# Kernel tuning notes

Hardware: AMD Instinct MI355X
Metric: run time of the kernel (lower is better)

Reference implementation:

```python
import jax, jax.numpy as jnp
import numpy as np

B, C, H, W = 8, 256, 128, 128
N = H * W
TEMP = 0.07
NUM_NEG = 128
HARD_RADIUS = 4
HARD_RATIO = 0.75   # curriculum fully ramped (_current_hard_ratio == hard_ratio_max)
N_HARD = int(NUM_NEG * HARD_RATIO)   # 96
N_RAND = NUM_NEG - N_HARD            # 32
STEP = max(1, H // 16)               # 8
N_POS = ((H + STEP - 1) // STEP) * ((W + STEP - 1) // STEP)  # 256


def setup_inputs() -> dict:
    key = jax.random.key(0)
    ks = jax.random.split(key, 8)
    fmap_rgb = jax.random.normal(ks[0], (B, C, H, W), jnp.float32)
    fmap_depth = jax.random.normal(ks[1], (B, C, H, W), jnp.float32)
    pu = jax.random.uniform(ks[2], (B, H, W), jnp.float32) * (W - 1)
    pv = jax.random.uniform(ks[3], (B, H, W), jnp.float32) * (H - 1)
    projected_coords = jnp.stack([pu, pv], axis=1)  # (B,2,H,W)
    valid_mask = (jax.random.uniform(ks[4], (B, H, W)) < 0.9).astype(jnp.float32)
    rand_idx = jax.random.randint(ks[5], (B, N_RAND), 0, N, dtype=jnp.int32)
    hard_off_u = jax.random.randint(ks[6], (B, N_HARD, N_POS), -HARD_RADIUS, HARD_RADIUS + 1, dtype=jnp.int32)
    hard_off_v = jax.random.randint(ks[7], (B, N_HARD, N_POS), -HARD_RADIUS, HARD_RADIUS + 1, dtype=jnp.int32)
    return {
        'fmap_rgb': fmap_rgb, 'fmap_depth': fmap_depth,
        'projected_coords': projected_coords, 'valid_mask': valid_mask,
        'rand_idx': rand_idx, 'hard_off_u': hard_off_u, 'hard_off_v': hard_off_v,
    }


def _normalize(x):
    # F.normalize(dim=1): x / max(||x||_2, eps)
    n = jnp.sqrt(jnp.sum(x * x, axis=1, keepdims=True))
    return x / jnp.maximum(n, 1e-12)


def _bilinear_sample(f, x, y):
    # grid_sample(mode=bilinear, padding=zeros, align_corners=True); unnormalized
    # coords equal pixel coords (x=proj_u, y=proj_v). f:(B,C,H,W), x,y:(B,H,W) -> (B,C,N)
    Bb, Cc, Hh, Ww = f.shape
    ff = f.reshape(Bb, Cc, Hh * Ww)
    xf = x.reshape(Bb, -1)
    yf = y.reshape(Bb, -1)
    x0 = jnp.floor(xf)
    y0 = jnp.floor(yf)
    wx = xf - x0
    wy = yf - y0
    x0i = x0.astype(jnp.int32)
    y0i = y0.astype(jnp.int32)

    def g(ix, iy):
        valid = (ix >= 0) & (ix < Ww) & (iy >= 0) & (iy < Hh)
        idx = jnp.clip(iy, 0, Hh - 1) * Ww + jnp.clip(ix, 0, Ww - 1)
        v = jnp.take_along_axis(ff, idx[:, None, :], axis=2)
        return v * valid[:, None, :]

    return (((1 - wx) * (1 - wy))[:, None, :] * g(x0i, y0i)
            + (wx * (1 - wy))[:, None, :] * g(x0i + 1, y0i)
            + ((1 - wx) * wy)[:, None, :] * g(x0i, y0i + 1)
            + (wx * wy)[:, None, :] * g(x0i + 1, y0i + 1))


def reference(fmap_rgb, fmap_depth, projected_coords, valid_mask, rand_idx, hard_off_u, hard_off_v):
    rgb = _normalize(fmap_rgb)
    dep = _normalize(fmap_depth)
    proj_u = projected_coords[:, 0]
    proj_v = projected_coords[:, 1]

    rgb_pos = _bilinear_sample(rgb, proj_u, proj_v)        # (B,C,N)
    dep_flat = dep.reshape(B, C, N)
    rgb_flat = rgb.reshape(B, C, N)
    pos_sim = jnp.sum(dep_flat * rgb_pos, axis=1) / TEMP    # (B,N)

    # random negatives via gather + batched matmul
    rgb_rand = jnp.take_along_axis(rgb_flat, rand_idx[:, None, :].astype(jnp.int32), axis=2)  # (B,C,n_rand)
    rand_neg = jnp.einsum('bcn,bck->bkn', dep_flat, rgb_rand) / TEMP  # (B,n_rand,N)

    # hard negatives on coarse grid (step = H//16)
    gh = jnp.arange(0, H, STEP)
    gw = jnp.arange(0, W, STEP)
    ghf, gwf = [a.reshape(-1) for a in jnp.meshgrid(gh, gw, indexing='ij')]
    grid_idx = ghf * W + gwf                                # (n_pos,)
    pos_u = jnp.clip(proj_u[:, ghf, gwf], 0, W - 1).astype(jnp.int32)  # (B,n_pos)
    pos_v = jnp.clip(proj_v[:, ghf, gwf], 0, H - 1).astype(jnp.int32)
    off_u = jnp.where((hard_off_u == 0) & (hard_off_v == 0), 1, hard_off_u)
    hu = jnp.clip(pos_u[:, None, :] + off_u, 0, W - 1)      # (B,n_hard,n_pos)
    hv = jnp.clip(pos_v[:, None, :] + hard_off_v, 0, H - 1)
    hard_idx = (hv * W + hu).reshape(B, -1)                 # (B, n_hard*n_pos)
    rgb_hard = jnp.take_along_axis(rgb_flat, hard_idx[:, None, :], axis=2).reshape(B, C, N_HARD, N_POS)
    dep_grid = dep_flat[:, :, grid_idx]                     # (B,C,n_pos)
    hard_sim = jnp.einsum('bcp,bchp->bhp', dep_grid, rgb_hard) / TEMP  # (B,n_hard,n_pos)

    # logsumexp over [pos; random negs; hard negs] -- hard negs only exist at grid
    # positions (the torch code scatters into a dense -inf (B,n_hard,N) tensor;
    # logaddexp at grid positions is mathematically identical and avoids it).
    lse_base = jax.scipy.special.logsumexp(
        jnp.concatenate([pos_sim[:, None, :], rand_neg], axis=1), axis=1)  # (B,N)
    lse_hard = jax.scipy.special.logsumexp(hard_sim, axis=1)               # (B,n_pos)
    lse = lse_base.at[:, grid_idx].set(jnp.logaddexp(lse_base[:, grid_idx], lse_hard))

    mask = valid_mask.reshape(B, N)
    denom = jnp.maximum(jnp.sum(mask), 1.0)
    loss = jnp.sum((lse - pos_sim) * mask) / denom

    # accuracy (no_grad in torch); max over all negatives, hard ones only at grid idx
    max_neg = jnp.max(rand_neg, axis=1)
    max_neg = max_neg.at[:, grid_idx].max(jnp.max(hard_sim, axis=1))
    correct = ((pos_sim > max_neg) & (mask > 0.5)).astype(jnp.float32)
    accuracy = jnp.sum(correct) / denom * 100.0
    return loss, jax.lax.stop_gradient(accuracy)
```

## Files before the change

### kernel.cpp

```cpp
#include <hip/hip_runtime.h>
#include <cfloat>
#include <math.h>

#define B_ 8
#define C_ 256
#define C2_ (C_/2)
#define H_ 128
#define W_ 128
#define N_ (H_*W_)
#define NRAND 32
#define NHARD 96
#define NPOS 256
#define INV_TEMP (1.0f/0.07f)

typedef __attribute__((ext_vector_type(8))) short short8;
typedef __attribute__((ext_vector_type(4))) float f32x4;

__device__ __forceinline__ unsigned bf16rne(float x) {
    unsigned u = __float_as_uint(x);
    return (u + 0x7FFFu + ((u >> 16) & 1u)) >> 16;
}
__device__ __forceinline__ float blo(unsigned w) { return __uint_as_float(w << 16); }
__device__ __forceinline__ float bhi(unsigned w) { return __uint_as_float(w & 0xFFFF0000u); }

__global__ __launch_bounds__(256) void k1_rgb_norm_T(const float* __restrict__ rgb,
                                                     unsigned* __restrict__ rgbT) {
    __shared__ float tile[C_][67];
    __shared__ float redx[8][32], redy[8][32];
    __shared__ float invn[64];
    int bi = blockIdx.x;
    int b  = bi >> 8;
    int p0 = (bi & 255) << 6;
    int t  = threadIdx.x;
    int pxh = t & 31;
    int cg  = t >> 5;
    const float2* src2 = (const float2*)(rgb + (size_t)b * C_ * N_);
    float ssx = 0.f, ssy = 0.f;
    #pragma unroll 4
    for (int p = 0; p < 32; ++p) {
        int c = p * 8 + cg;
        float2 v = src2[(size_t)c * (N_ / 2) + (p0 >> 1) + pxh];
        tile[c][2 * pxh]     = v.x;
        tile[c][2 * pxh + 1] = v.y;
        ssx += v.x * v.x;
        ssy += v.y * v.y;
    }
    redx[cg][pxh] = ssx; redy[cg][pxh] = ssy;
    __syncthreads();
    if (t < 32) {
        float sx = 0.f, sy = 0.f;
        #pragma unroll
        for (int g2 = 0; g2 < 8; ++g2) { sx += redx[g2][t]; sy += redy[g2][t]; }
        invn[2 * t]     = 1.0f / fmaxf(sqrtf(sx), 1e-12f);
        invn[2 * t + 1] = 1.0f / fmaxf(sqrtf(sy), 1e-12f);
    }
    __syncthreads();
    unsigned* dst = rgbT + (size_t)(b * N_ + p0) * C2_;
    int u  = t & 127;
    int ph = t >> 7;
    #pragma unroll 4
    for (int it = 0; it < 32; ++it) {
        int px = ph + 2 * it;
        float sc = invn[px];
        unsigned pa = bf16rne(tile[2 * u][px] * sc);
        unsigned pb = bf16rne(tile[2 * u + 1][px] * sc);
        dst[(size_t)px * C2_ + u] = pa | (pb << 16);
    }
}

__global__ __launch_bounds__(256) void k2_main(
        const float* __restrict__ dep, const unsigned* __restrict__ rgbT,
        const float* __restrict__ coords, const int* __restrict__ rand_idx,
        float* __restrict__ lse_base, float* __restrict__ pos_out,
        float* __restrict__ maxneg_out, unsigned* __restrict__ depG) {
    __shared__ __align__(16) uint4 dep4[64 * 32];
    __shared__ __align__(16) uint4 rs4[32 * 32];
    __shared__ float red[4][64];
    __shared__ float invn[64];
    int bi = blockIdx.x;
    int b  = bi >> 8;
    int p0 = (bi & 255) << 6;
    int t  = threadIdx.x;
    int lane = t & 63, w = t >> 6;

    #pragma unroll
    for (int it = 0; it < 4; ++it) {
        int flat = it * 256 + t;
        int rn = flat >> 5, c8 = flat & 31;
        int idx = rand_idx[b * NRAND + rn];
        const uint4* src = (const uint4*)(rgbT + (size_t)(b * N_ + idx) * C2_);
        rs4[rn * 32 + (c8 ^ (rn & 7))] = src[c8];
    }

    const float* depb = dep + (size_t)b * C_ * N_ + p0 + lane;
    float ssq = 0.f;
    int psw = lane & 7;
    #pragma unroll 2
    for (int i = 0; i < 8; ++i) {
        int c0 = w * 64 + i * 8;
        float v[8];
        #pragma unroll
        for (int k = 0; k < 8; ++k) {
            v[k] = depb[(size_t)(c0 + k) * N_];
            ssq += v[k] * v[k];
        }
        uint4 q;
        q.x = bf16rne(v[0]) | (bf16rne(v[1]) << 16);
        q.y = bf16rne(v[2]) | (bf16rne(v[3]) << 16);
        q.z = bf16rne(v[4]) | (bf16rne(v[5]) << 16);
        q.w = bf16rne(v[6]) | (bf16rne(v[7]) << 16);
        dep4[lane * 32 + ((w * 8 + i) ^ psw)] = q;
    }
    red[w][lane] = ssq;

    int px = t >> 2, g = t & 3;
    int n  = p0 + px;
    float xf = coords[(size_t)b * 2 * N_ + n];
    float yf = coords[(size_t)b * 2 * N_ + N_ + n];
    float x0 = floorf(xf), y0 = floorf(yf);
    float wx = xf - x0, wy = yf - y0;
    int ix = (int)x0 + (g & 1);
    int iy = (int)y0 + (g >> 1);
    float wgt = ((g & 1) ? wx : 1.f - wx) * ((g & 2) ? wy : 1.f - wy);
    if (ix < 0 || ix >= W_ || iy < 0 || iy >= H_) wgt = 0.f;
    int ixc = min(max(ix, 0), W_ - 1), iyc = min(max(iy, 0), H_ - 1);
    const uint4* nbr4 = (const uint4*)(rgbT + (size_t)(b * N_ + iyc * W_ + ixc) * C2_);

    __syncthreads();
    if (t < 64) {
        float s = red[0][t] + red[1][t] + red[2][t] + red[3][t];
        invn[t] = 1.0f / fmaxf(sqrtf(s), 1e-12f);
    }

    f32x4 acc0 = {0.f, 0.f, 0.f, 0.f};
    f32x4 acc1 = {0.f, 0.f, 0.f, 0.f};
    int l15 = lane & 15, l4 = lane >> 4;
    int pxA = (w << 4) + l15;
    const short8* lds8 = (const short8*)dep4;
    const short8* rnd8 = (const short8*)rs4;
    #pragma unroll
    for (int kc = 0; kc < 8; ++kc) {
        int c8 = kc * 4 + l4;
        short8 a  = lds8[pxA * 32 + (c8 ^ (pxA & 7))];
        short8 b0 = rnd8[l15 * 32 + (c8 ^ (l15 & 7))];
        short8 b1 = rnd8[(16 + l15) * 32 + (c8 ^ (l15 & 7))];
        acc0 = __builtin_amdgcn_mfma_f32_16x16x32_bf16(a, b0, acc0, 0, 0, 0);
        acc1 = __builtin_amdgcn_mfma_f32_16x16x32_bf16(a, b1, acc1, 0, 0, 0);
    }

    float accN = 0.f;
    const uint4* drow = dep4 + (size_t)px * 32;
    int dsw = px & 7;
    #pragma unroll 4
    for (int c8 = 0; c8 < 32; ++c8) {
        uint4 dq = drow[c8 ^ dsw];
        uint4 rq = nbr4[c8];
        accN += blo(dq.x) * blo(rq.x) + bhi(dq.x) * bhi(rq.x)
              + blo(dq.y) * blo(rq.y) + bhi(dq.y) * bhi(rq.y)
              + blo(dq.z) * blo(rq.z) + bhi(dq.z) * bhi(rq.z)
              + blo(dq.w) * blo(rq.w) + bhi(dq.w) * bhi(rq.w);
    }
    __syncthreads();

    float* simsF = (float*)rs4;
    #pragma unroll
    for (int r = 0; r < 4; ++r) {
        int prow = (w << 4) + (l4 << 2) + r;
        int swn = r << 2;
        simsF[prow * 32 + (l15 ^ swn)]        = acc0[r];
        simsF[prow * 32 + (16 + (l15 ^ swn))] = acc1[r];
    }
    __syncthreads();

    float scale = invn[px] * INV_TEMP;
    float pp = accN * wgt;
    pp += __shfl_xor(pp, 1, 4);
    pp += __shfl_xor(pp, 2, 4);
    float pos = pp * scale;
    const float4* sf = (const float4*)simsF;
    int fsw = px & 3;
    float4 ra = sf[px * 8 + ((g * 2) ^ fsw)];
    float4 rb = sf[px * 8 + (((g * 2) ^ fsw) ^ 1)];
    float r[8] = {ra.x, ra.y, ra.z, ra.w, rb.x, rb.y, rb.z, rb.w};
    float ml = -FLT_MAX;
    #pragma unroll
    for (int j = 0; j < 8; ++j) { r[j] *= scale; ml = fmaxf(ml, r[j]); }
    ml = fmaxf(ml, __shfl_xor(ml, 1, 4));
    ml = fmaxf(ml, __shfl_xor(ml, 2, 4));
    float mneg = ml;
    float mall = fmaxf(mneg, pos);
    float se = 0.f;
    #pragma unroll
    for (int j = 0; j < 8; ++j) se += expf(r[j] - mall);
    se += __shfl_xor(se, 1, 4);
    se += __shfl_xor(se, 2, 4);
    if (g == 0) {
        float lse = mall + logf(se + expf(pos - mall));
        size_t o = (size_t)b * N_ + n;
        lse_base[o]   = lse;
        pos_out[o]    = pos;
        maxneg_out[o] = mneg;
    }

    int y = p0 >> 7;
    if ((y & 7) == 0) {
        int m = t >> 5, u = t & 31;
        int gpx = m * 8;
        int gx  = (p0 & 127) + gpx;
        int p   = ((y >> 3) << 4) + (gx >> 3);
        float sc = invn[gpx];
        const unsigned* srow = (const unsigned*)(dep4 + (size_t)gpx * 32);
        int xsw = (gpx & 7) << 2;
        unsigned* dst = depG + (size_t)((b << 8) + p) * 128;
        #pragma unroll
        for (int it = 0; it < 4; ++it) {
            int uu = u + it * 32;
            unsigned wv = srow[uu ^ xsw];
            dst[uu] = bf16rne(blo(wv) * sc) | (bf16rne(bhi(wv) * sc) << 16);
        }
    }
}

__global__ __launch_bounds__(128) void k3_hard(
        const unsigned* __restrict__ depG, const unsigned* __restrict__ rgbT,
        const float* __restrict__ coords, const int* __restrict__ hoffu,
        const int* __restrict__ hoffv, float* __restrict__ lse_hard,
        float* __restrict__ max_hard) {
    __shared__ __align__(16) float dv[256];
    __shared__ float sm_[2], ss_[2];
    int bp = blockIdx.x;
    int b = bp >> 8, p = bp & 255;
    int gy = (p >> 4) * 8, gx = (p & 15) * 8;
    int nn = gy * W_ + gx;
    int t  = threadIdx.x;
    unsigned wv = depG[(size_t)bp * 128 + t];
    dv[2 * t]     = blo(wv);
    dv[2 * t + 1] = bhi(wv);
    float pu = coords[(size_t)b * 2 * N_ + nn];
    float pv = coords[(size_t)b * 2 * N_ + N_ + nn];
    int iu = (int)fminf(fmaxf(pu, 0.f), (float)(W_ - 1));
    int iv = (int)fminf(fmaxf(pv, 0.f), (float)(H_ - 1));
    float sim = -FLT_MAX;
    int ou = 0, ov = 0;
    if (t < NHARD) {
        ou = hoffu[((size_t)b * NHARD + t) * NPOS + p];
        ov = hoffv[((size_t)b * NHARD + t) * NPOS + p];
    }
    __syncthreads();
    if (t < NHARD) {
        if (ou == 0 && ov == 0) ou = 1;
        int hu = min(max(iu + ou, 0), W_ - 1);
        int hv = min(max(iv + ov, 0), H_ - 1);
        const uint4* hvec = (const uint4*)(rgbT + (size_t)(b * N_ + hv * W_ + hu) * C2_);
        float acc = 0.f;
        #pragma unroll 4
        for (int c8 = 0; c8 < 32; ++c8) {
            uint4 q = hvec[c8];
            float4 d0 = *(const float4*)(&dv[c8 * 8]);
            float4 d1 = *(const float4*)(&dv[c8 * 8 + 4]);
            acc += d0.x * blo(q.x) + d0.y * bhi(q.x)
                 + d0.z * blo(q.y) + d0.w * bhi(q.y)
                 + d1.x * blo(q.z) + d1.y * bhi(q.z)
                 + d1.z * blo(q.w) + d1.w * bhi(q.w);
        }
        sim = acc * INV_TEMP;
    }
    float m = sim;
    #pragma unroll
    for (int o = 32; o > 0; o >>= 1) m = fmaxf(m, __shfl_down(m, o, 64));
    int wid = t >> 6;
    if ((t & 63) == 0) sm_[wid] = m;
    __syncthreads();
    float mm = fmaxf(sm_[0], sm_[1]);
    float e = (t < NHARD) ? expf(sim - mm) : 0.f;
    #pragma unroll
    for (int o = 32; o > 0; o >>= 1) e += __shfl_down(e, o, 64);
    if ((t & 63) == 0) ss_[wid] = e;
    __syncthreads();
    if (t == 0) {
        lse_hard[bp] = mm + logf(ss_[0] + ss_[1]);
        max_hard[bp] = mm;
    }
}

__global__ __launch_bounds__(256) void k4_reduce(
        const float* __restrict__ lse_base, const float* __restrict__ pos_sim,
        const float* __restrict__ max_neg, const float* __restrict__ mask,
        const float* __restrict__ lse_hard, const float* __restrict__ max_hard,
        float* __restrict__ acc) {
    int i = blockIdx.x * 256 + threadIdx.x;
    float l  = lse_base[i], ps = pos_sim[i], mn = max_neg[i], mk = mask[i];
    int b = i >> 14;
    int n = i & (N_ - 1);
    int y = n >> 7, x = n & 127;
    if (((y & 7) | (x & 7)) == 0) {
        int p = ((y >> 3) << 4) + (x >> 3);
        float lh = lse_hard[(b << 8) + p];
        float mh = max_hard[(b << 8) + p];
        float m = fmaxf(l, lh);
        l  = m + logf(expf(l - m) + expf(lh - m));
        mn = fmaxf(mn, mh);
    }
    float s0 = (l - ps) * mk;
    float s1 = (ps > mn && mk > 0.5f) ? 1.f : 0.f;
    float s2 = mk;
    #pragma unroll
    for (int o = 32; o > 0; o >>= 1) {
        s0 += __shfl_down(s0, o, 64);
        s1 += __shfl_down(s1, o, 64);
        s2 += __shfl_down(s2, o, 64);
    }
    __shared__ float r0[4], r1[4], r2[4];
    int wid = threadIdx.x >> 6;
    if ((threadIdx.x & 63) == 0) { r0[wid] = s0; r1[wid] = s1; r2[wid] = s2; }
    __syncthreads();
    if (threadIdx.x == 0) {
        atomicAdd(&acc[0], r0[0] + r0[1] + r0[2] + r0[3]);
        atomicAdd(&acc[1], r1[0] + r1[1] + r1[2] + r1[3]);
        atomicAdd(&acc[2], r2[0] + r2[1] + r2[2] + r2[3]);
    }
}

__global__ void k5_final(const float* __restrict__ acc, float* __restrict__ out) {
    if (threadIdx.x == 0) {
        float denom = fmaxf(acc[2], 1.0f);
        out[0] = acc[0] / denom;
        out[1] = acc[1] / denom * 100.0f;
    }
}

extern "C" void kernel_launch(void* const* d_in, const int* in_sizes, int n_in,
                              void* d_out, int out_size, void* d_ws, size_t ws_size,
                              hipStream_t stream) {
    const float* rgb     = (const float*)d_in[0];
    const float* dep     = (const float*)d_in[1];
    const float* coords  = (const float*)d_in[2];
    const float* mask    = (const float*)d_in[3];
    const int*   rand_i  = (const int*)d_in[4];
    const int*   hoffu   = (const int*)d_in[5];
    const int*   hoffv   = (const int*)d_in[6];
    float* out = (float*)d_out;
    char*  ws  = (char*)d_ws;

    const size_t RGBT_B = (size_t)B_ * N_ * C_ * 2;
    const size_t PIX_B  = (size_t)B_ * N_ * 4;
    unsigned* rgbT  = (unsigned*)ws;
    float* lse_base = (float*)(ws + RGBT_B);
    float* pos_sim  = (float*)(ws + RGBT_B + PIX_B);
    float* max_neg  = (float*)(ws + RGBT_B + 2 * PIX_B);
    float* lse_hard = (float*)(ws + RGBT_B + 3 * PIX_B);
    float* max_hard = (float*)(ws + RGBT_B + 3 * PIX_B + 8192);
    float* acc      = (float*)(ws + RGBT_B + 3 * PIX_B + 2 * 8192);
    unsigned* depG  = (unsigned*)(ws + RGBT_B + 3 * PIX_B + 2 * 8192 + 1024);

    hipMemsetAsync(acc, 0, 16, stream);
    k1_rgb_norm_T<<<B_ * (N_ / 64), 256, 0, stream>>>(rgb, rgbT);
    k2_main<<<B_ * (N_ / 64), 256, 0, stream>>>(dep, rgbT, coords, rand_i,
                                                lse_base, pos_sim, max_neg, depG);
    k3_hard<<<B_ * NPOS, 128, 0, stream>>>(depG, rgbT, coords, hoffu, hoffv,
                                           lse_hard, max_hard);
    k4_reduce<<<(B_ * N_) / 256, 256, 0, stream>>>(lse_base, pos_sim, max_neg,
                                                   mask, lse_hard, max_hard, acc);
    k5_final<<<1, 64, 0, stream>>>(acc, out);
}
```

Before: 370.4 us.

## Register-staged rgb normalize with swizzled LDS transpose; split hard dot over thread pairs

The rgb normalize/transpose kernel now loads 64 channels per thread into registers with coalesced per-channel reads. It packs bf16 pairs into uint4 and stages them through an XOR-swizzled LDS buffer so rows of 16-byte chunks can be written to global memory. This replaces the padded float tile and scalar 4-byte stores. The hard-negative kernel uses 192 threads, with two threads per hard negative each computing half of the 256-channel dot product and combining via a shuffle. That removes the idle lanes of the old 96-of-128 layout and shortens each thread's gather chain, at the cost of heavy register use (64 floats per thread) in k1.

New measurement: 371.8 us. No clear change (+0.4%).

```diff
diff --git a/kernel.cpp b/kernel.cpp
--- a/kernel.cpp
+++ b/kernel.cpp
@@ -25,46 +25,48 @@
 
 __global__ __launch_bounds__(256) void k1_rgb_norm_T(const float* __restrict__ rgb,
                                                      unsigned* __restrict__ rgbT) {
-    __shared__ float tile[C_][67];
-    __shared__ float redx[8][32], redy[8][32];
+    __shared__ __align__(16) uint4 bounce[64 * 32];
+    __shared__ float red[4][64];
     __shared__ float invn[64];
     int bi = blockIdx.x;
     int b  = bi >> 8;
     int p0 = (bi & 255) << 6;
     int t  = threadIdx.x;
-    int pxh = t & 31;
-    int cg  = t >> 5;
-    const float2* src2 = (const float2*)(rgb + (size_t)b * C_ * N_);
-    float ssx = 0.f, ssy = 0.f;
-    #pragma unroll 4
-    for (int p = 0; p < 32; ++p) {
-        int c = p * 8 + cg;
-        float2 v = src2[(size_t)c * (N_ / 2) + (p0 >> 1) + pxh];
-        tile[c][2 * pxh]     = v.x;
-        tile[c][2 * pxh + 1] = v.y;
-        ssx += v.x * v.x;
-        ssy += v.y * v.y;
-    }
-    redx[cg][pxh] = ssx; redy[cg][pxh] = ssy;
-    __syncthreads();
-    if (t < 32) {
-        float sx = 0.f, sy = 0.f;
-        #pragma unroll
-        for (int g2 = 0; g2 < 8; ++g2) { sx += redx[g2][t]; sy += redy[g2][t]; }
-        invn[2 * t]     = 1.0f / fmaxf(sqrtf(sx), 1e-12f);
-        invn[2 * t + 1] = 1.0f / fmaxf(sqrtf(sy), 1e-12f);
-    }
-    __syncthreads();
-    unsigned* dst = rgbT + (size_t)(b * N_ + p0) * C2_;
-    int u  = t & 127;
-    int ph = t >> 7;
-    #pragma unroll 4
-    for (int it = 0; it < 32; ++it) {
-        int px = ph + 2 * it;
-        float sc = invn[px];
-        unsigned pa = bf16rne(tile[2 * u][px] * sc);
-        unsigned pb = bf16rne(tile[2 * u + 1][px] * sc);
-        dst[(size_t)px * C2_ + u] = pa | (pb << 16);
+    int lane = t & 63, w = t >> 6;
+
+    const float* src = rgb + (size_t)b * C_ * N_ + p0 + lane;
+    float v[64];
+    float ssq = 0.f;
+    #pragma unroll
+    for (int k = 0; k < 64; ++k) {
+        v[k] = src[(size_t)(w * 64 + k) * N_];
+        ssq += v[k] * v[k];
+    }
+    red[w][lane] = ssq;
+    __syncthreads();
+    if (t < 64) {
+        float s = red[0][t] + red[1][t] + red[2][t] + red[3][t];
+        invn[t] = 1.0f / fmaxf(sqrtf(s), 1e-12f);
+    }
+    __syncthreads();
+    float sc = invn[lane];
+    int swz = lane & 7;
+    #pragma unroll
+    for (int j = 0; j < 8; ++j) {
+        uint4 q;
+        q.x = bf16rne(v[8 * j + 0] * sc) | (bf16rne(v[8 * j + 1] * sc) << 16);
+        q.y = bf16rne(v[8 * j + 2] * sc) | (bf16rne(v[8 * j + 3] * sc) << 16);
+        q.z = bf16rne(v[8 * j + 4] * sc) | (bf16rne(v[8 * j + 5] * sc) << 16);
+        q.w = bf16rne(v[8 * j + 6] * sc) | (bf16rne(v[8 * j + 7] * sc) << 16);
+        bounce[lane * 32 + ((w * 8 + j) ^ swz)] = q;
+    }
+    __syncthreads();
+    uint4* dst = (uint4*)(rgbT + (size_t)(b * N_ + p0) * C2_);
+    #pragma unroll
+    for (int it = 0; it < 8; ++it) {
+        int idx = it * 256 + t;
+        int px = idx >> 5, j = idx & 31;
+        dst[idx] = bounce[px * 32 + (j ^ (px & 7))];
     }
 }
 
@@ -221,64 +223,63 @@
     }
 }
 
-__global__ __launch_bounds__(128) void k3_hard(
+__global__ __launch_bounds__(192) void k3_hard(
         const unsigned* __restrict__ depG, const unsigned* __restrict__ rgbT,
         const float* __restrict__ coords, const int* __restrict__ hoffu,
         const int* __restrict__ hoffv, float* __restrict__ lse_hard,
         float* __restrict__ max_hard) {
     __shared__ __align__(16) float dv[256];
-    __shared__ float sm_[2], ss_[2];
+    __shared__ float sm_[3], ss_[3];
     int bp = blockIdx.x;
     int b = bp >> 8, p = bp & 255;
     int gy = (p >> 4) * 8, gx = (p & 15) * 8;
     int nn = gy * W_ + gx;
     int t  = threadIdx.x;
-    unsigned wv = depG[(size_t)bp * 128 + t];
-    dv[2 * t]     = blo(wv);
-    dv[2 * t + 1] = bhi(wv);
+    if (t < 128) {
+        unsigned wv = depG[(size_t)bp * 128 + t];
+        dv[2 * t]     = blo(wv);
+        dv[2 * t + 1] = bhi(wv);
+    }
     float pu = coords[(size_t)b * 2 * N_ + nn];
     float pv = coords[(size_t)b * 2 * N_ + N_ + nn];
     int iu = (int)fminf(fmaxf(pu, 0.f), (float)(W_ - 1));
     int iv = (int)fminf(fmaxf(pv, 0.f), (float)(H_ - 1));
-    float sim = -FLT_MAX;
-    int ou = 0, ov = 0;
-    if (t < NHARD) {
-        ou = hoffu[((size_t)b * NHARD + t) * NPOS + p];
-        ov = hoffv[((size_t)b * NHARD + t) * NPOS + p];
-    }
-    __syncthreads();
-    if (t < NHARD) {
-        if (ou == 0 && ov == 0) ou = 1;
-        int hu = min(max(iu + ou, 0), W_ - 1);
-        int hv = min(max(iv + ov, 0), H_ - 1);
-        const uint4* hvec = (const uint4*)(rgbT + (size_t)(b * N_ + hv * W_ + hu) * C2_);
-        float acc = 0.f;
-        #pragma unroll 4
-        for (int c8 = 0; c8 < 32; ++c8) {
-            uint4 q = hvec[c8];
-            float4 d0 = *(const float4*)(&dv[c8 * 8]);
-            float4 d1 = *(const float4*)(&dv[c8 * 8 + 4]);
-            acc += d0.x * blo(q.x) + d0.y * bhi(q.x)
-                 + d0.z * blo(q.y) + d0.w * bhi(q.y)
-                 + d1.x * blo(q.z) + d1.y * bhi(q.z)
-                 + d1.z * blo(q.w) + d1.w * bhi(q.w);
-        }
-        sim = acc * INV_TEMP;
-    }
+    int h = t >> 1, half = t & 1;
+    int ou = hoffu[((size_t)b * NHARD + h) * NPOS + p];
+    int ov = hoffv[((size_t)b * NHARD + h) * NPOS + p];
+    __syncthreads();
+    if (ou == 0 && ov == 0) ou = 1;
+    int hu = min(max(iu + ou, 0), W_ - 1);
+    int hv = min(max(iv + ov, 0), H_ - 1);
+    const uint4* hvec = (const uint4*)(rgbT + (size_t)(b * N_ + hv * W_ + hu) * C2_)
+                        + half * 16;
+    const float4* dvv = (const float4*)dv + half * 32;
+    float acc = 0.f;
+    #pragma unroll 4
+    for (int c8 = 0; c8 < 16; ++c8) {
+        uint4 q = hvec[c8];
+        float4 d0 = dvv[c8 * 2];
+        float4 d1 = dvv[c8 * 2 + 1];
+        acc += d0.x * blo(q.x) + d0.y * bhi(q.x)
+             + d0.z * blo(q.y) + d0.w * bhi(q.y)
+             + d1.x * blo(q.z) + d1.y * bhi(q.z)
+             + d1.z * blo(q.w) + d1.w * bhi(q.w);
+    }
+    float sim = (acc + __shfl_xor(acc, 1, 2)) * INV_TEMP;
     float m = sim;
     #pragma unroll
-    for (int o = 32; o > 0; o >>= 1) m = fmaxf(m, __shfl_down(m, o, 64));
+    for (int o = 32; o > 0; o >>= 1) m = fmaxf(m, __shfl_xor(m, o, 64));
     int wid = t >> 6;
     if ((t & 63) == 0) sm_[wid] = m;
     __syncthreads();
-    float mm = fmaxf(sm_[0], sm_[1]);
-    float e = (t < NHARD) ? expf(sim - mm) : 0.f;
-    #pragma unroll
-    for (int o = 32; o > 0; o >>= 1) e += __shfl_down(e, o, 64);
+    float mm = fmaxf(fmaxf(sm_[0], sm_[1]), sm_[2]);
+    float e = (half == 0) ? expf(sim - mm) : 0.f;
+    #pragma unroll
+    for (int o = 32; o > 0; o >>= 1) e += __shfl_xor(e, o, 64);
     if ((t & 63) == 0) ss_[wid] = e;
     __syncthreads();
     if (t == 0) {
-        lse_hard[bp] = mm + logf(ss_[0] + ss_[1]);
+        lse_hard[bp] = mm + logf(ss_[0] + ss_[1] + ss_[2]);
         max_hard[bp] = mm;
     }
 }
@@ -357,7 +358,7 @@
     k1_rgb_norm_T<<<B_ * (N_ / 64), 256, 0, stream>>>(rgb, rgbT);
     k2_main<<<B_ * (N_ / 64), 256, 0, stream>>>(dep, rgbT, coords, rand_i,
                                                 lse_base, pos_sim, max_neg, depG);
-    k3_hard<<<B_ * NPOS, 128, 0, stream>>>(depG, rgbT, coords, hoffu, hoffv,
+    k3_hard<<<B_ * NPOS, 192, 0, stream>>>(depG, rgbT, coords, hoffu, hoffv,
                                            lse_hard, max_hard);
     k4_reduce<<<(B_ * N_) / 256, 256, 0, stream>>>(lse_base, pos_sim, max_neg,
                                                    mask, lse_hard, max_hard, acc);
```
